# Kernel optimization log

Measured on AMD Instinct MI355X. Metric: run time of the kernel, lower is better.

The kernel has to match this reference:

```python
import jax, jax.numpy as jnp
import numpy as np

B, S, D_IN, D_OUT, RANK = 4, 2048, 4096, 4096, 16
SCALING = 32.0 / RANK  # alpha / rank
MASK_DENSITY = 0.01


def setup_inputs() -> dict:
    key = jax.random.key(0)
    ks = jax.random.split(key, 7)
    x = jax.random.normal(ks[0], (B, S, D_IN), dtype=jnp.float32)
    W = jax.random.normal(ks[1], (D_OUT, D_IN), dtype=jnp.float32) / np.sqrt(D_IN)
    b = jax.random.normal(ks[2], (D_OUT,), dtype=jnp.float32) * 0.01
    lora_A = jax.random.normal(ks[3], (RANK, D_IN), dtype=jnp.float32) / np.sqrt(D_IN)
    lora_B = jax.random.normal(ks[4], (D_OUT, RANK), dtype=jnp.float32) * 0.01
    delta = jax.random.normal(ks[5], (D_OUT, D_IN), dtype=jnp.float32) * 0.01
    mask = jax.random.bernoulli(ks[6], MASK_DENSITY, (D_OUT, D_IN))
    return {"x": x, "W": W, "b": b, "lora_A": lora_A, "lora_B": lora_B,
            "delta": delta, "mask": mask}


def reference(x, W, b, lora_A, lora_B, delta, mask):
    # frozen linear: [B,S,D_in] @ [D_in,D_out] + b
    out = jnp.einsum("bsd,od->bso", x, W) + b
    # LoRA branch: (x @ A^T) @ B^T * scaling
    out = out + jnp.einsum("bsr,or->bso", jnp.einsum("bsd,rd->bsr", x, lora_A), lora_B) * SCALING
    # sparse delta branch: F.linear(x, delta * mask)
    masked_delta = delta * mask.astype(delta.dtype)
    out = out + jnp.einsum("bsd,od->bso", x, masked_delta)
    return out
```

## Files before the change

### kernel.cpp

```cpp
#include <hip/hip_runtime.h>
#include <hip/hip_bf16.h>

typedef __hip_bfloat16 bf16;
typedef __attribute__((ext_vector_type(8))) short bf16x8;
typedef __attribute__((ext_vector_type(4))) float f32x4;
typedef __attribute__((ext_vector_type(4))) int int4v;

#define AS1 __attribute__((address_space(1)))
#define AS3 __attribute__((address_space(3)))

#define MDIM 8192
#define NDIM 4096
#define KDIM 4096
#define SCALING 2.0f

__global__ __launch_bounds__(256) void prep(
    const float* __restrict__ W, const float* __restrict__ lA,
    const float* __restrict__ lB, const float* __restrict__ delta,
    const int* __restrict__ mask, bf16* __restrict__ Weff,
    const float* __restrict__ X, bf16* __restrict__ Xb)
{
    const int bid = blockIdx.x;
    const int tid = threadIdx.x;

    if (bid < 2048) {
        const int ob    = (bid >> 3) * 16;
        const int db    = (bid & 7) * 512;
        const int obase = ob + (tid >> 6) * 4;
        const int dc    = db + (tid & 63) * 8;

        float Bo[4][16];
#pragma unroll
        for (int oo = 0; oo < 4; ++oo)
#pragma unroll
            for (int r = 0; r < 16; ++r)
                Bo[oo][r] = lB[(obase + oo) * 16 + r];

        float lor[4][8];
#pragma unroll
        for (int oo = 0; oo < 4; ++oo)
#pragma unroll
            for (int e = 0; e < 8; ++e) lor[oo][e] = 0.f;

#pragma unroll
        for (int r = 0; r < 16; ++r) {
            f32x4 aa = *(const f32x4*)(lA + (size_t)r * KDIM + dc);
            f32x4 ab = *(const f32x4*)(lA + (size_t)r * KDIM + dc + 4);
#pragma unroll
            for (int oo = 0; oo < 4; ++oo)
#pragma unroll
                for (int e = 0; e < 4; ++e) {
                    lor[oo][e]     += Bo[oo][r] * aa[e];
                    lor[oo][e + 4] += Bo[oo][r] * ab[e];
                }
        }

#pragma unroll
        for (int oo = 0; oo < 4; ++oo) {
            const size_t base = (size_t)(obase + oo) * KDIM + dc;

            f32x4 wa  = *(const f32x4*)(W + base);
            f32x4 wb  = *(const f32x4*)(W + base + 4);
            f32x4 da  = *(const f32x4*)(delta + base);
            f32x4 db4 = *(const f32x4*)(delta + base + 4);

            int mk[8];
            *(int4v*)(mk)     = *(const int4v*)(mask + base);
            *(int4v*)(mk + 4) = *(const int4v*)(mask + base + 4);

            int4v ov4;
            bf16* ov = (bf16*)&ov4;
#pragma unroll
            for (int e = 0; e < 8; ++e) {
                float w = (e < 4) ? wa[e] : wb[e - 4];
                float d = (e < 4) ? da[e] : db4[e - 4];
                float a = w + SCALING * lor[oo][e];
                if (mk[e]) a += d;
                ov[e] = __float2bfloat16(a);
            }
            *(int4v*)(Weff + base) = ov4;
        }
    } else {
        const size_t nchunk = (size_t)MDIM * KDIM / 8;
        for (size_t c = (size_t)(bid - 2048) * 256 + tid; c < nchunk;
             c += (size_t)2048 * 256) {
            const size_t i = c * 8;
            f32x4 a = *(const f32x4*)(X + i);
            f32x4 b = *(const f32x4*)(X + i + 4);
            int4v ov4;
            bf16* ov = (bf16*)&ov4;
#pragma unroll
            for (int e = 0; e < 4; ++e) {
                ov[e]     = __float2bfloat16(a[e]);
                ov[e + 4] = __float2bfloat16(b[e]);
            }
            *(int4v*)(Xb + i) = ov4;
        }
    }
}

__global__ __launch_bounds__(256, 4) void gemm_bf16(
    const bf16* __restrict__ X, const bf16* __restrict__ Wt,
    const float* __restrict__ bias, float* __restrict__ out)
{
    __shared__ bf16 As[128 * 64];
    __shared__ bf16 Bs[128 * 64];

    const int tid  = threadIdx.x;
    const int lane = tid & 63;
    const int wave = tid >> 6;
    const int wm   = wave & 1;
    const int wn   = wave >> 1;
    const int quad = lane >> 4;
    const int l16  = lane & 15;

    const int bn = blockIdx.x * 128;
    const int bm = blockIdx.y * 128;
    const int cwave = tid & ~63;

    f32x4 acc[4][4];
#pragma unroll
    for (int i = 0; i < 4; ++i)
#pragma unroll
        for (int j = 0; j < 4; ++j)
            acc[i][j] = (f32x4){0.f, 0.f, 0.f, 0.f};

    for (int kt = 0; kt < KDIM / 64; ++kt) {
        const int k0 = kt * 64;
        if (kt) __syncthreads();
#pragma unroll
        for (int j = 0; j < 4; ++j) {
            const int c  = j * 256 + tid;
            const int m  = c >> 3;
            const int kc = (c & 7) ^ (m & 7);
            const int cb = j * 256 + cwave;
            __builtin_amdgcn_global_load_lds(
                (const AS1 void*)(X + (size_t)(bm + m) * KDIM + k0 + kc * 8),
                (AS3 void*)(As + cb * 8), 16, 0, 0);
            __builtin_amdgcn_global_load_lds(
                (const AS1 void*)(Wt + (size_t)(bn + m) * KDIM + k0 + kc * 8),
                (AS3 void*)(Bs + cb * 8), 16, 0, 0);
        }
        __syncthreads();

#pragma unroll
        for (int ks = 0; ks < 2; ++ks) {
            bf16x8 af[4], bfr[4];
#pragma unroll
            for (int i = 0; i < 4; ++i) {
                const int m   = wm * 64 + i * 16 + l16;
                const int kca = (ks * 4 + quad) ^ (m & 7);
                af[i] = *(const bf16x8*)(As + m * 64 + kca * 8);
                const int n   = wn * 64 + i * 16 + l16;
                const int kcb = (ks * 4 + quad) ^ (n & 7);
                bfr[i] = *(const bf16x8*)(Bs + n * 64 + kcb * 8);
            }
#pragma unroll
            for (int i = 0; i < 4; ++i)
#pragma unroll
                for (int j = 0; j < 4; ++j)
                    acc[i][j] = __builtin_amdgcn_mfma_f32_16x16x32_bf16(
                        af[i], bfr[j], acc[i][j], 0, 0, 0);
        }
    }

    float bv[4];
#pragma unroll
    for (int j = 0; j < 4; ++j)
        bv[j] = bias[bn + wn * 64 + j * 16 + l16];

#pragma unroll
    for (int i = 0; i < 4; ++i) {
        const int mg = bm + wm * 64 + i * 16 + quad * 4;
#pragma unroll
        for (int j = 0; j < 4; ++j) {
            const int ng = bn + wn * 64 + j * 16 + l16;
#pragma unroll
            for (int r = 0; r < 4; ++r)
                out[(size_t)(mg + r) * NDIM + ng] = acc[i][j][r] + bv[j];
        }
    }
}

__global__ __launch_bounds__(256, 3) void gemm_f32(
    const float* __restrict__ X, const bf16* __restrict__ Wt,
    const float* __restrict__ bias, float* __restrict__ out)
{
    __shared__ float Asf[128 * 64];
    __shared__ bf16  Bs[128 * 64];

    const int tid  = threadIdx.x;
    const int lane = tid & 63;
    const int wave = tid >> 6;
    const int wmf  = wave & 1;
    const int wnf  = wave >> 1;
    const int quad = lane >> 4;
    const int l16  = lane & 15;

    const int bn = blockIdx.x * 128;
    const int bm = blockIdx.y * 128;
    const int cwave = tid & ~63;

    f32x4 acc[4][4];
#pragma unroll
    for (int i = 0; i < 4; ++i)
#pragma unroll
        for (int j = 0; j < 4; ++j)
            acc[i][j] = (f32x4){0.f, 0.f, 0.f, 0.f};

    for (int kt = 0; kt < KDIM / 64; ++kt) {
        const int k0 = kt * 64;
        if (kt) __syncthreads();
#pragma unroll
        for (int j = 0; j < 8; ++j) {
            const int c  = j * 256 + tid;
            const int m  = c >> 4;
            const int kc = (c & 15) ^ (m & 15);
            const int cb = j * 256 + cwave;
            __builtin_amdgcn_global_load_lds(
                (const AS1 void*)(X + (size_t)(bm + m) * KDIM + k0 + kc * 4),
                (AS3 void*)(Asf + cb * 4), 16, 0, 0);
        }
#pragma unroll
        for (int j = 0; j < 4; ++j) {
            const int c  = j * 256 + tid;
            const int m  = c >> 3;
            const int kc = (c & 7) ^ (m & 7);
            const int cb = j * 256 + cwave;
            __builtin_amdgcn_global_load_lds(
                (const AS1 void*)(Wt + (size_t)(bn + m) * KDIM + k0 + kc * 8),
                (AS3 void*)(Bs + cb * 8), 16, 0, 0);
        }
        __syncthreads();

#pragma unroll
        for (int ks = 0; ks < 2; ++ks) {
            bf16x8 af[4], bfr[4];
#pragma unroll
            for (int i = 0; i < 4; ++i) {
                const int m  = wmf * 64 + i * 16 + l16;
                const int k2 = (ks * 4 + quad) * 2;
                f32x4 lo = *(const f32x4*)(Asf + m * 64 + ((k2     ^ (m & 15)) * 4));
                f32x4 hi = *(const f32x4*)(Asf + m * 64 + (((k2+1) ^ (m & 15)) * 4));
                bf16 tmp[8];
#pragma unroll
                for (int e = 0; e < 4; ++e) {
                    tmp[e]     = __float2bfloat16(lo[e]);
                    tmp[e + 4] = __float2bfloat16(hi[e]);
                }
                af[i] = *(const bf16x8*)tmp;

                const int n   = wnf * 64 + i * 16 + l16;
                const int kcb = (ks * 4 + quad) ^ (n & 7);
                bfr[i] = *(const bf16x8*)(Bs + n * 64 + kcb * 8);
            }
#pragma unroll
            for (int i = 0; i < 4; ++i)
#pragma unroll
                for (int j = 0; j < 4; ++j)
                    acc[i][j] = __builtin_amdgcn_mfma_f32_16x16x32_bf16(
                        af[i], bfr[j], acc[i][j], 0, 0, 0);
        }
    }

    float bv[4];
#pragma unroll
    for (int j = 0; j < 4; ++j)
        bv[j] = bias[bn + wnf * 64 + j * 16 + l16];

#pragma unroll
    for (int i = 0; i < 4; ++i) {
        const int mg = bm + wmf * 64 + i * 16 + quad * 4;
#pragma unroll
        for (int j = 0; j < 4; ++j) {
            const int ng = bn + wnf * 64 + j * 16 + l16;
#pragma unroll
            for (int r = 0; r < 4; ++r)
                out[(size_t)(mg + r) * NDIM + ng] = acc[i][j][r] + bv[j];
        }
    }
}

extern "C" void kernel_launch(void* const* d_in, const int* in_sizes, int n_in,
                              void* d_out, int out_size, void* d_ws, size_t ws_size,
                              hipStream_t stream)
{
    const float* x     = (const float*)d_in[0];
    const float* W     = (const float*)d_in[1];
    const float* b     = (const float*)d_in[2];
    const float* lA    = (const float*)d_in[3];
    const float* lB    = (const float*)d_in[4];
    const float* delta = (const float*)d_in[5];
    const int*   mask  = (const int*)d_in[6];
    float* out = (float*)d_out;

    bf16* Weff = (bf16*)d_ws;
    bf16* Xb   = (bf16*)((char*)d_ws + (size_t)NDIM * KDIM * 2);

    const size_t need = (size_t)NDIM * KDIM * 2 + (size_t)MDIM * KDIM * 2;

    if (ws_size >= need) {
        prep<<<dim3(4096), 256, 0, stream>>>(
            W, lA, lB, delta, mask, Weff, x, Xb);
        gemm_bf16<<<dim3(NDIM / 128, MDIM / 128), 256, 0, stream>>>(
            Xb, Weff, b, out);
    } else {
        prep<<<dim3(2048), 256, 0, stream>>>(
            W, lA, lB, delta, mask, Weff, x, Xb);
        gemm_f32<<<dim3(NDIM / 128, MDIM / 128), 256, 0, stream>>>(
            x, Weff, b, out);
    }
}
```

Measured before the change: 610.4 us.

## Double-buffer LDS tiles and use 8 waves per block in bf16 GEMM

The bf16 GEMM now keeps two LDS buffers for each of the A and B tiles and issues the global-to-LDS loads for the next k-tile before computing on the current one, with a single barrier per iteration. The block grows from 256 to 512 threads, so each wave covers a 64x32 output sub-tile instead of 64x64. The goal is to hide global load latency behind MFMA work and add waves per CU. The cost is double the LDS per block (64 KB), which together with the 512-thread launch bound may limit how many blocks fit on a CU. Each wave also does less MFMA work per LDS fragment load.

```diff
diff --git a/kernel.cpp b/kernel.cpp
--- a/kernel.cpp
+++ b/kernel.cpp
@@ -13,6 +13,7 @@
 #define NDIM 4096
 #define KDIM 4096
 #define SCALING 2.0f
+#define NT (KDIM / 64)
 
 __global__ __launch_bounds__(256) void prep(
     const float* __restrict__ W, const float* __restrict__ lA,
@@ -99,15 +100,16 @@
     }
 }
 
-__global__ __launch_bounds__(256, 4) void gemm_bf16(
+__global__ __launch_bounds__(512, 4) void gemm_bf16(
     const bf16* __restrict__ X, const bf16* __restrict__ Wt,
     const float* __restrict__ bias, float* __restrict__ out)
 {
-    __shared__ bf16 As[128 * 64];
-    __shared__ bf16 Bs[128 * 64];
+    __shared__ bf16 As[2][128 * 64];
+    __shared__ bf16 Bs[2][128 * 64];
 
     const int tid  = threadIdx.x;
     const int lane = tid & 63;
+    const int wvb  = tid & ~63;
     const int wave = tid >> 6;
     const int wm   = wave & 1;
     const int wn   = wave >> 1;
@@ -116,70 +118,85 @@
 
     const int bn = blockIdx.x * 128;
     const int bm = blockIdx.y * 128;
-    const int cwave = tid & ~63;
-
-    f32x4 acc[4][4];
+
+    f32x4 acc[4][2];
 #pragma unroll
     for (int i = 0; i < 4; ++i)
 #pragma unroll
-        for (int j = 0; j < 4; ++j)
+        for (int j = 0; j < 2; ++j)
             acc[i][j] = (f32x4){0.f, 0.f, 0.f, 0.f};
 
-    for (int kt = 0; kt < KDIM / 64; ++kt) {
-        const int k0 = kt * 64;
-        if (kt) __syncthreads();
-#pragma unroll
-        for (int j = 0; j < 4; ++j) {
-            const int c  = j * 256 + tid;
-            const int m  = c >> 3;
-            const int kc = (c & 7) ^ (m & 7);
-            const int cb = j * 256 + cwave;
-            __builtin_amdgcn_global_load_lds(
-                (const AS1 void*)(X + (size_t)(bm + m) * KDIM + k0 + kc * 8),
-                (AS3 void*)(As + cb * 8), 16, 0, 0);
-            __builtin_amdgcn_global_load_lds(
-                (const AS1 void*)(Wt + (size_t)(bn + m) * KDIM + k0 + kc * 8),
-                (AS3 void*)(Bs + cb * 8), 16, 0, 0);
-        }
-        __syncthreads();
-
+#define STAGE(buf, kt)                                                         \
+    {                                                                          \
+        const int k0_ = (kt) * 64;                                             \
+        _Pragma("unroll")                                                      \
+        for (int gi = 0; gi < 2; ++gi) {                                       \
+            const int c  = gi * 512 + tid;                                     \
+            const int m  = c >> 3;                                             \
+            const int kc = (c & 7) ^ (m & 7);                                  \
+            const int cb = gi * 512 + wvb;                                     \
+            __builtin_amdgcn_global_load_lds(                                  \
+                (const AS1 void*)(X + (size_t)(bm + m) * KDIM + k0_ + kc * 8), \
+                (AS3 void*)(As[buf] + cb * 8), 16, 0, 0);                      \
+            __builtin_amdgcn_global_load_lds(                                  \
+                (const AS1 void*)(Wt + (size_t)(bn + m) * KDIM + k0_ + kc * 8),\
+                (AS3 void*)(Bs[buf] + cb * 8), 16, 0, 0);                      \
+        }                                                                      \
+    }
+
+    STAGE(0, 0)
+    __syncthreads();
+
+    for (int kt = 0; kt < NT; ++kt) {
+        const int cur = kt & 1;
+
+        if (kt + 1 < NT) STAGE(cur ^ 1, kt + 1)
+
+        const bf16* Ac = As[cur];
+        const bf16* Bc = Bs[cur];
 #pragma unroll
         for (int ks = 0; ks < 2; ++ks) {
-            bf16x8 af[4], bfr[4];
+            bf16x8 af[4], bfr[2];
 #pragma unroll
             for (int i = 0; i < 4; ++i) {
                 const int m   = wm * 64 + i * 16 + l16;
                 const int kca = (ks * 4 + quad) ^ (m & 7);
-                af[i] = *(const bf16x8*)(As + m * 64 + kca * 8);
-                const int n   = wn * 64 + i * 16 + l16;
+                af[i] = *(const bf16x8*)(Ac + m * 64 + kca * 8);
+            }
+#pragma unroll
+            for (int j = 0; j < 2; ++j) {
+                const int n   = wn * 32 + j * 16 + l16;
                 const int kcb = (ks * 4 + quad) ^ (n & 7);
-                bfr[i] = *(const bf16x8*)(Bs + n * 64 + kcb * 8);
+                bfr[j] = *(const bf16x8*)(Bc + n * 64 + kcb * 8);
             }
 #pragma unroll
             for (int i = 0; i < 4; ++i)
 #pragma unroll
-                for (int j = 0; j < 4; ++j)
+                for (int j = 0; j < 2; ++j)
                     acc[i][j] = __builtin_amdgcn_mfma_f32_16x16x32_bf16(
                         af[i], bfr[j], acc[i][j], 0, 0, 0);
         }
-    }
-
-    float bv[4];
-#pragma unroll
-    for (int j = 0; j < 4; ++j)
-        bv[j] = bias[bn + wn * 64 + j * 16 + l16];
+
+        __syncthreads();
+    }
+
+    float bv[2];
+#pragma unroll
+    for (int j = 0; j < 2; ++j)
+        bv[j] = bias[bn + wn * 32 + j * 16 + l16];
 
 #pragma unroll
     for (int i = 0; i < 4; ++i) {
         const int mg = bm + wm * 64 + i * 16 + quad * 4;
 #pragma unroll
-        for (int j = 0; j < 4; ++j) {
-            const int ng = bn + wn * 64 + j * 16 + l16;
+        for (int j = 0; j < 2; ++j) {
+            const int ng = bn + wn * 32 + j * 16 + l16;
 #pragma unroll
             for (int r = 0; r < 4; ++r)
                 out[(size_t)(mg + r) * NDIM + ng] = acc[i][j][r] + bv[j];
         }
     }
+#undef STAGE
 }
 
 __global__ __launch_bounds__(256, 3) void gemm_f32(
@@ -302,7 +319,7 @@
     if (ws_size >= need) {
         prep<<<dim3(4096), 256, 0, stream>>>(
             W, lA, lB, delta, mask, Weff, x, Xb);
-        gemm_bf16<<<dim3(NDIM / 128, MDIM / 128), 256, 0, stream>>>(
+        gemm_bf16<<<dim3(NDIM / 128, MDIM / 128), 512, 0, stream>>>(
             Xb, Weff, b, out);
     } else {
         prep<<<dim3(2048), 256, 0, stream>>>(
```

New measurement: 639.7 us. 1.05x slower.
